# Optimization experiments

Hardware: AMD Instinct MI355X
Metric: run time of the kernel (lower is better)

## Reference

```python
import jax, jax.numpy as jnp
import numpy as np

BS, N, D, H = 4, 2048, 512, 8
DK = D // H
XAVIER_STD = float(np.sqrt(2.0 / (D + D)))  # xavier_normal_, gain=1


def setup_inputs() -> dict:
    key = jax.random.key(0)
    ks = jax.random.split(key, 10)
    Q = jax.random.normal(ks[0], (BS, N, D), jnp.float32)
    K = jax.random.normal(ks[1], (BS, N, D), jnp.float32)
    V = jax.random.normal(ks[2], (BS, N, D), jnp.float32)
    q_mas = jax.random.randint(ks[3], (BS, N, 1), 0, 2).astype(jnp.float32)
    k_mas = jax.random.randint(ks[4], (BS, N, 1), 0, 2).astype(jnp.float32)
    # 0/1 attention mask; force self-edges so no row is fully masked (avoids NaN softmax)
    att_mas = jax.random.randint(ks[5], (BS, N, N), 0, 2).astype(jnp.float32)
    att_mas = jnp.maximum(att_mas, jnp.eye(N, dtype=jnp.float32)[None])
    WQ = jax.random.normal(ks[6], (D, D), jnp.float32) * XAVIER_STD
    WK = jax.random.normal(ks[7], (D, D), jnp.float32) * XAVIER_STD
    WV = jax.random.normal(ks[8], (D, D), jnp.float32) * XAVIER_STD
    WO = jax.random.normal(ks[9], (D, D), jnp.float32) * XAVIER_STD
    return {"Q": Q, "K": K, "V": V, "q_mas": q_mas, "k_mas": k_mas,
            "att_mas": att_mas, "WQ": WQ, "WK": WK, "WV": WV, "WO": WO}


def reference(Q, K, V, q_mas, k_mas, att_mas, WQ, WK, WV, WO):
    bs, n, d = Q.shape
    h, dk = H, DK
    qm = q_mas.reshape(bs, 1, n, 1)  # (bs,1,n,1)
    km = k_mas.reshape(bs, 1, n, 1)
    # nn.Linear (no bias): x @ W.T ; split heads -> (bs,h,n,dk); apply pre-masks
    Qh = qm * (Q @ WQ.T).reshape(bs, n, h, dk).transpose(0, 2, 1, 3)
    Kh = km * (K @ WK.T).reshape(bs, n, h, dk).transpose(0, 2, 1, 3)
    Vh = km * (V @ WV.T).reshape(bs, n, h, dk).transpose(0, 2, 1, 3)
    scores = jnp.einsum('bhqd,bhkd->bhqk', Qh, Kh) / jnp.sqrt(jnp.float32(dk))
    mas = att_mas.reshape(bs, 1, n, n)
    scores = jnp.where(mas.astype(bool), scores, -jnp.inf)
    attn = jax.nn.softmax(scores, axis=-1) * mas
    y = jnp.einsum('bhqk,bhkd->bhqd', attn, Vh) * km  # post-mask (note: km over query dim, as in source)
    y = y.transpose(0, 2, 1, 3).reshape(bs, n, d)
    y = (y @ WO.T) * k_mas.reshape(bs, n, 1)
    return y
```

## Files before the change

kernel.cpp:

```cpp
#include <hip/hip_runtime.h>


#define BS_    4
#define NSEQ   2048
#define DMODEL 512
#define NH     8
#define DKH    64
#define MROWS  (BS_ * NSEQ)

typedef unsigned short ushort_t;
typedef __attribute__((ext_vector_type(8))) short short8;
typedef __attribute__((ext_vector_type(4))) float floatx4;

__device__ __forceinline__ ushort_t f2bf(float f) {
    unsigned int x = __builtin_bit_cast(unsigned int, f);
    return (ushort_t)((x + 0x8000u) >> 16);
}
__device__ __forceinline__ floatx4 mfma_bf16(short8 a, short8 b, floatx4 c) {
    return __builtin_amdgcn_mfma_f32_16x16x32_bf16(a, b, c, 0, 0, 0);
}
__device__ __forceinline__ void gld16(const ushort_t* g, ushort_t* l) {
    __builtin_amdgcn_global_load_lds(
        (const __attribute__((address_space(1))) unsigned int*)g,
        (__attribute__((address_space(3))) unsigned int*)l, 16, 0, 0);
}

__global__ __launch_bounds__(256) void cvt3_kernel(const float* __restrict__ a,
                                                   const float* __restrict__ b,
                                                   const float* __restrict__ c,
                                                   ushort_t* __restrict__ dst, int n4) {
    const float* src = (blockIdx.y == 0) ? a : (blockIdx.y == 1) ? b : c;
    ushort_t* d = dst + (size_t)blockIdx.y * ((size_t)n4 * 4);
    const int i = blockIdx.x * blockDim.x + threadIdx.x;
    const float4 v = ((const float4*)src)[i];
    ushort4 o;
    o.x = f2bf(v.x); o.y = f2bf(v.y); o.z = f2bf(v.z); o.w = f2bf(v.w);
    ((ushort4*)d)[i] = o;
}

__global__ __launch_bounds__(256) void cvt4_kernel(const float* __restrict__ a,
                                                   const float* __restrict__ b,
                                                   const float* __restrict__ c,
                                                   const float* __restrict__ e,
                                                   ushort_t* __restrict__ dst, int n4) {
    const float* src = (blockIdx.y == 0) ? a : (blockIdx.y == 1) ? b
                     : (blockIdx.y == 2) ? c : e;
    ushort_t* d = dst + (size_t)blockIdx.y * ((size_t)n4 * 4);
    const int i = blockIdx.x * blockDim.x + threadIdx.x;
    const float4 v = ((const float4*)src)[i];
    ushort4 o;
    o.x = f2bf(v.x); o.y = f2bf(v.y); o.z = f2bf(v.z); o.w = f2bf(v.w);
    ((ushort4*)d)[i] = o;
}

__global__ __launch_bounds__(256) void gemm_proj(const ushort_t* __restrict__ Xall,
                                                 const ushort_t* __restrict__ Wall,
                                                 const float* __restrict__ qmas,
                                                 const float* __restrict__ kmas,
                                                 ushort_t* __restrict__ Qh,
                                                 ushort_t* __restrict__ Kh,
                                                 ushort_t* __restrict__ Vt) {
    __shared__ ushort_t As[2][128 * 32];
    const int z = blockIdx.z;
    const ushort_t* X  = Xall + (size_t)z * MROWS * DMODEL;
    const ushort_t* Wb = Wall + (size_t)z * DMODEL * DMODEL;
    const float* rowmask = (z == 0) ? qmas : kmas;

    const int tid  = threadIdx.x;
    const int wave = tid >> 6;
    const int lane = tid & 63;
    const int l16  = lane & 15;
    const int quad = lane >> 4;
    const int wr   = wave >> 1;
    const int wc   = wave & 1;
    const int m0   = blockIdx.x * 128;
    const int n0   = blockIdx.y * 128;
    const int r4   = lane >> 2;
    const int p4   = lane & 3;

    floatx4 acc[4][4];
#pragma unroll
    for (int t = 0; t < 4; ++t)
#pragma unroll
        for (int u = 0; u < 4; ++u) acc[t][u] = (floatx4){0.f, 0.f, 0.f, 0.f};

    const ushort_t* Wrow[4];
#pragma unroll
    for (int u = 0; u < 4; ++u)
        Wrow[u] = Wb + (size_t)(n0 + wc * 64 + u * 16 + l16) * DMODEL + quad * 8;

    for (int k0 = 0; k0 < DMODEL; k0 += 64) {
#pragma unroll
        for (int i = 0; i < 4; ++i) {
            const int idx = wave * 4 + i;
            const int h = idx >> 3, rg = idx & 7;
            gld16(X + (size_t)(m0 + rg * 16 + r4) * DMODEL + k0 + h * 32 + p4 * 8,
                  &As[h][rg * 512]);
        }
        short8 bf[4][2];
#pragma unroll
        for (int u = 0; u < 4; ++u)
#pragma unroll
            for (int kc = 0; kc < 2; ++kc)
                bf[u][kc] = *(const short8*)(Wrow[u] + k0 + kc * 32);
        __syncthreads();
        short8 af[4][2];
#pragma unroll
        for (int t = 0; t < 4; ++t)
#pragma unroll
            for (int kc = 0; kc < 2; ++kc)
                af[t][kc] = *(const short8*)&As[kc][(wr * 64 + t * 16 + l16) * 32 + quad * 8];
#pragma unroll
        for (int t = 0; t < 4; ++t)
#pragma unroll
            for (int u = 0; u < 4; ++u) {
                acc[t][u] = mfma_bf16(af[t][0], bf[u][0], acc[t][u]);
                acc[t][u] = mfma_bf16(af[t][1], bf[u][1], acc[t][u]);
            }
        __syncthreads();
    }

    float rm[4][4];
#pragma unroll
    for (int t = 0; t < 4; ++t)
#pragma unroll
        for (int r = 0; r < 4; ++r)
            rm[t][r] = rowmask[m0 + wr * 64 + t * 16 + quad * 4 + r];

    const int bb    = m0 >> 11;
    const int nbase = (m0 & (NSEQ - 1)) + wr * 64;
#pragma unroll
    for (int t = 0; t < 4; ++t) {
#pragma unroll
        for (int u = 0; u < 4; ++u) {
            const int d = n0 + wc * 64 + u * 16 + l16;
            const int h = d >> 6, cc = d & 63;
            if (z < 2) {
                ushort_t* dst = (z == 0) ? Qh : Kh;
#pragma unroll
                for (int r = 0; r < 4; ++r) {
                    const int n = nbase + t * 16 + quad * 4 + r;
                    dst[((size_t)(bb * NH + h) * NSEQ + n) * DKH + cc] =
                        f2bf(acc[t][u][r] * rm[t][r]);
                }
            } else {
                ushort4 pk;
                pk.x = f2bf(acc[t][u][0] * rm[t][0]);
                pk.y = f2bf(acc[t][u][1] * rm[t][1]);
                pk.z = f2bf(acc[t][u][2] * rm[t][2]);
                pk.w = f2bf(acc[t][u][3] * rm[t][3]);
                const int n = nbase + t * 16 + quad * 4;
                *(ushort4*)(Vt + ((size_t)(bb * NH + h) * DKH + cc) * NSEQ + n) = pk;
            }
        }
    }
}

__global__ __launch_bounds__(256) void gemm_out(const ushort_t* __restrict__ X,
                                                const ushort_t* __restrict__ Wb,
                                                const float* __restrict__ rowmask,
                                                float* __restrict__ dst) {
    __shared__ ushort_t As[2][128 * 32];
    const int tid  = threadIdx.x;
    const int wave = tid >> 6;
    const int lane = tid & 63;
    const int l16  = lane & 15;
    const int quad = lane >> 4;
    const int wr   = wave >> 1;
    const int wc   = wave & 1;
    const int m0   = blockIdx.x * 128;
    const int n0   = blockIdx.y * 128;
    const int r4   = lane >> 2;
    const int p4   = lane & 3;

    floatx4 acc[4][4];
#pragma unroll
    for (int t = 0; t < 4; ++t)
#pragma unroll
        for (int u = 0; u < 4; ++u) acc[t][u] = (floatx4){0.f, 0.f, 0.f, 0.f};

    const ushort_t* Wrow[4];
#pragma unroll
    for (int u = 0; u < 4; ++u)
        Wrow[u] = Wb + (size_t)(n0 + wc * 64 + u * 16 + l16) * DMODEL + quad * 8;

    for (int k0 = 0; k0 < DMODEL; k0 += 64) {
#pragma unroll
        for (int i = 0; i < 4; ++i) {
            const int idx = wave * 4 + i;
            const int h = idx >> 3, rg = idx & 7;
            gld16(X + (size_t)(m0 + rg * 16 + r4) * DMODEL + k0 + h * 32 + p4 * 8,
                  &As[h][rg * 512]);
        }
        short8 bf[4][2];
#pragma unroll
        for (int u = 0; u < 4; ++u)
#pragma unroll
            for (int kc = 0; kc < 2; ++kc)
                bf[u][kc] = *(const short8*)(Wrow[u] + k0 + kc * 32);
        __syncthreads();
        short8 af[4][2];
#pragma unroll
        for (int t = 0; t < 4; ++t)
#pragma unroll
            for (int kc = 0; kc < 2; ++kc)
                af[t][kc] = *(const short8*)&As[kc][(wr * 64 + t * 16 + l16) * 32 + quad * 8];
#pragma unroll
        for (int t = 0; t < 4; ++t)
#pragma unroll
            for (int u = 0; u < 4; ++u) {
                acc[t][u] = mfma_bf16(af[t][0], bf[u][0], acc[t][u]);
                acc[t][u] = mfma_bf16(af[t][1], bf[u][1], acc[t][u]);
            }
        __syncthreads();
    }

#pragma unroll
    for (int t = 0; t < 4; ++t) {
#pragma unroll
        for (int r = 0; r < 4; ++r) {
            const int m = m0 + wr * 64 + t * 16 + quad * 4 + r;
            const float rm = rowmask[m];
#pragma unroll
            for (int u = 0; u < 4; ++u) {
                const int d = n0 + wc * 64 + u * 16 + l16;
                dst[(size_t)m * DMODEL + d] = acc[t][u][r] * rm;
            }
        }
    }
}

__global__ __launch_bounds__(256, 3) void attn_kernel(const ushort_t* __restrict__ Qh,
                                                      const ushort_t* __restrict__ Kh,
                                                      const ushort_t* __restrict__ Vt,
                                                      const float* __restrict__ amas,
                                                      const float* __restrict__ kmas,
                                                      ushort_t* __restrict__ y) {
    __shared__ ushort_t Ks[2][128 * 32];
    __shared__ ushort_t Vs[4][64 * 32];
    __shared__ ushort_t Ps[4][4][16 * 32];

    const int tid  = threadIdx.x;
    const int wave = tid >> 6;
    const int lane = tid & 63;
    const int l16  = lane & 15;
    const int quad = lane >> 4;
    const int r4   = lane >> 2;
    const int p4   = lane & 3;
    const int h    = blockIdx.y;
    const int b    = blockIdx.z;
    const int qw   = blockIdx.x * 64 + wave * 16;

    const ushort_t* Kb = Kh + (size_t)(b * NH + h) * NSEQ * DKH;
    const ushort_t* Vb = Vt + (size_t)(b * NH + h) * DKH * NSEQ;
    const float*    Am = amas + (size_t)(b * NSEQ + qw) * NSEQ;

    const ushort_t* Qp = Qh + ((size_t)((b * NH + h) * NSEQ) + qw + l16) * DKH + quad * 8;
    const short8 qfa = *(const short8*)Qp;
    const short8 qfb = *(const short8*)(Qp + 32);

    float lpart[4] = {0.f, 0.f, 0.f, 0.f};
    floatx4 accO[4];
#pragma unroll
    for (int ct = 0; ct < 4; ++ct) accO[ct] = (floatx4){0.f, 0.f, 0.f, 0.f};

    const float CEXP = 0.18033688011112042f;

    for (int kt = 0; kt < NSEQ / 128; ++kt) {
        const int k0 = kt * 128;

        __syncthreads();

        float av[8][4];
#pragma unroll
        for (int fr = 0; fr < 8; ++fr)
#pragma unroll
            for (int r = 0; r < 4; ++r)
                av[fr][r] = Am[(size_t)(quad * 4 + r) * NSEQ + k0 + fr * 16 + l16];

#pragma unroll
        for (int i = 0; i < 4; ++i) {
            const int idx = wave * 4 + i;
            const int hh = idx >> 3, rg = idx & 7;
            gld16(Kb + (size_t)(k0 + rg * 16 + r4) * DKH + hh * 32 + p4 * 8,
                  &Ks[hh][rg * 512]);
        }
#pragma unroll
        for (int i = 0; i < 4; ++i) {
            const int idx = wave * 4 + i;
            const int kf = idx >> 2, rg = idx & 3;
            gld16(Vb + (size_t)(rg * 16 + r4) * NSEQ + k0 + kf * 32 + p4 * 8,
                  &Vs[kf][rg * 512]);
        }
        __syncthreads();

        floatx4 S[8];
#pragma unroll
        for (int fr = 0; fr < 8; ++fr) {
            const short8 ka = *(const short8*)&Ks[0][(fr * 16 + l16) * 32 + quad * 8];
            const short8 kb = *(const short8*)&Ks[1][(fr * 16 + l16) * 32 + quad * 8];
            floatx4 s = {0.f, 0.f, 0.f, 0.f};
            s = mfma_bf16(qfa, ka, s);
            s = mfma_bf16(qfb, kb, s);
            S[fr] = s;
        }

#pragma unroll
        for (int fr = 0; fr < 8; ++fr) {
#pragma unroll
            for (int r = 0; r < 4; ++r) {
                const float p = av[fr][r] * exp2f(S[fr][r] * CEXP);
                lpart[r] += p;
                Ps[wave][fr >> 1][(quad * 4 + r) * 32 + (fr & 1) * 16 + l16] = f2bf(p);
            }
        }

        __builtin_amdgcn_wave_barrier();
        short8 pf[4];
#pragma unroll
        for (int kf = 0; kf < 4; ++kf)
            pf[kf] = *(const short8*)&Ps[wave][kf][l16 * 32 + quad * 8];
        __builtin_amdgcn_wave_barrier();

#pragma unroll
        for (int ct = 0; ct < 4; ++ct) {
#pragma unroll
            for (int kf = 0; kf < 4; ++kf) {
                const short8 vb = *(const short8*)&Vs[kf][(ct * 16 + l16) * 32 + quad * 8];
                accO[ct] = mfma_bf16(pf[kf], vb, accO[ct]);
            }
        }
    }

#pragma unroll
    for (int r = 0; r < 4; ++r) {
        float l = lpart[r];
        l += __shfl_xor(l, 1);
        l += __shfl_xor(l, 2);
        l += __shfl_xor(l, 4);
        l += __shfl_xor(l, 8);
        const int q = qw + quad * 4 + r;
        const float scale = kmas[b * NSEQ + q] / l;
#pragma unroll
        for (int ct = 0; ct < 4; ++ct) {
            y[(size_t)(b * NSEQ + q) * DMODEL + h * DKH + ct * 16 + l16] =
                f2bf(accO[ct][r] * scale);
        }
    }
}

extern "C" void kernel_launch(void* const* d_in, const int* in_sizes, int n_in,
                              void* d_out, int out_size, void* d_ws, size_t ws_size,
                              hipStream_t stream) {
    (void)in_sizes; (void)n_in; (void)out_size; (void)ws_size;
    const float* Q  = (const float*)d_in[0];
    const float* K  = (const float*)d_in[1];
    const float* V  = (const float*)d_in[2];
    const float* qm = (const float*)d_in[3];
    const float* km = (const float*)d_in[4];
    const float* am = (const float*)d_in[5];
    const float* WQ = (const float*)d_in[6];
    const float* WK = (const float*)d_in[7];
    const float* WV = (const float*)d_in[8];
    const float* WO = (const float*)d_in[9];

    const size_t XN = (size_t)MROWS * DMODEL;
    const size_t WN = (size_t)DMODEL * DMODEL;
    ushort_t* Xbf = (ushort_t*)d_ws;
    ushort_t* Wbf = Xbf + 3 * XN;
    ushort_t* WOb = Wbf + 3 * WN;
    ushort_t* Qh  = Wbf + 4 * WN;
    ushort_t* Kh  = Qh + XN;
    ushort_t* Vt  = Kh + XN;
    ushort_t* y   = Vt + XN;
    float* out = (float*)d_out;

    hipLaunchKernelGGL(cvt3_kernel, dim3(4096, 3), dim3(256), 0, stream,
                       Q, K, V, Xbf, (int)(XN / 4));
    hipLaunchKernelGGL(cvt4_kernel, dim3(256, 4), dim3(256), 0, stream,
                       WQ, WK, WV, WO, Wbf, (int)(WN / 4));

    hipLaunchKernelGGL(gemm_proj, dim3(MROWS / 128, DMODEL / 128, 3), dim3(256), 0, stream,
                       Xbf, Wbf, qm, km, Qh, Kh, Vt);

    hipLaunchKernelGGL(attn_kernel, dim3(NSEQ / 64, NH, BS_), dim3(256), 0, stream,
                       Qh, Kh, Vt, am, km, y);

    hipLaunchKernelGGL(gemm_out, dim3(MROWS / 128, DMODEL / 128), dim3(256), 0, stream,
                       y, WOb, km, out);
}
```

Before: 294.2 us.

## Bit-pack attention mask, merge conversion kernels, retile GEMMs with LDS-staged weights

A single prep kernel now does the bf16 conversions of inputs and weights and also packs the float attention mask into a 1-bit-per-entry bitmask using wave ballots. The attention kernel then reads 32x less mask data. It also swaps the MFMA operand order so each lane holds one query row, which allows packed bf16 P stores and a simpler row-sum reduction through LDS. The projection and output GEMMs move to 64x128 tiles with weights staged in LDS via global_load_lds, giving more blocks and less register pressure. The cost is one extra full pass over the float mask in the prep kernel.

```diff
diff --git a/kernel.cpp b/kernel.cpp
--- a/kernel.cpp
+++ b/kernel.cpp
@@ -7,6 +7,9 @@
 #define NH     8
 #define DKH    64
 #define MROWS  (BS_ * NSEQ)
+#define NW32   (NSEQ / 32)
+#define XN     ((size_t)MROWS * DMODEL)
+#define WN     ((size_t)DMODEL * DMODEL)
 
 typedef unsigned short ushort_t;
 typedef __attribute__((ext_vector_type(8))) short short8;
@@ -15,6 +18,11 @@
 __device__ __forceinline__ ushort_t f2bf(float f) {
     unsigned int x = __builtin_bit_cast(unsigned int, f);
     return (ushort_t)((x + 0x8000u) >> 16);
+}
+__device__ __forceinline__ unsigned int pack2bf(float lo, float hi) {
+    const unsigned int a = __builtin_bit_cast(unsigned int, lo) + 0x8000u;
+    const unsigned int b = __builtin_bit_cast(unsigned int, hi) + 0x8000u;
+    return __builtin_amdgcn_perm(b, a, 0x07060302u);
 }
 __device__ __forceinline__ floatx4 mfma_bf16(short8 a, short8 b, floatx4 c) {
     return __builtin_amdgcn_mfma_f32_16x16x32_bf16(a, b, c, 0, 0, 0);
@@ -25,33 +33,78 @@
         (__attribute__((address_space(3))) unsigned int*)l, 16, 0, 0);
 }
 
-__global__ __launch_bounds__(256) void cvt3_kernel(const float* __restrict__ a,
-                                                   const float* __restrict__ b,
-                                                   const float* __restrict__ c,
-                                                   ushort_t* __restrict__ dst, int n4) {
-    const float* src = (blockIdx.y == 0) ? a : (blockIdx.y == 1) ? b : c;
-    ushort_t* d = dst + (size_t)blockIdx.y * ((size_t)n4 * 4);
-    const int i = blockIdx.x * blockDim.x + threadIdx.x;
-    const float4 v = ((const float4*)src)[i];
-    ushort4 o;
-    o.x = f2bf(v.x); o.y = f2bf(v.y); o.z = f2bf(v.z); o.w = f2bf(v.w);
-    ((ushort4*)d)[i] = o;
-}
-
-__global__ __launch_bounds__(256) void cvt4_kernel(const float* __restrict__ a,
-                                                   const float* __restrict__ b,
-                                                   const float* __restrict__ c,
-                                                   const float* __restrict__ e,
-                                                   ushort_t* __restrict__ dst, int n4) {
-    const float* src = (blockIdx.y == 0) ? a : (blockIdx.y == 1) ? b
-                     : (blockIdx.y == 2) ? c : e;
-    ushort_t* d = dst + (size_t)blockIdx.y * ((size_t)n4 * 4);
-    const int i = blockIdx.x * blockDim.x + threadIdx.x;
-    const float4 v = ((const float4*)src)[i];
-    ushort4 o;
-    o.x = f2bf(v.x); o.y = f2bf(v.y); o.z = f2bf(v.z); o.w = f2bf(v.w);
-    ((ushort4*)d)[i] = o;
-}
+__global__ __launch_bounds__(256) void prep_kernel(const float* __restrict__ Q,
+                                                   const float* __restrict__ K,
+                                                   const float* __restrict__ V,
+                                                   const float* __restrict__ WQ,
+                                                   const float* __restrict__ WK,
+                                                   const float* __restrict__ WV,
+                                                   const float* __restrict__ WO,
+                                                   const float* __restrict__ am,
+                                                   ushort_t* __restrict__ Xbf,
+                                                   ushort_t* __restrict__ Wbf,
+                                                   unsigned int* __restrict__ pm) {
+    const int bx  = blockIdx.x;
+    const int tid = threadIdx.x;
+    if (bx < 12288) {
+        const int seg = bx >> 12;
+        const int i = (bx & 4095) * 256 + tid;
+        const float* src = (seg == 0) ? Q : (seg == 1) ? K : V;
+        const float4 v = ((const float4*)src)[i];
+        ushort4 o;
+        o.x = f2bf(v.x); o.y = f2bf(v.y); o.z = f2bf(v.z); o.w = f2bf(v.w);
+        ((ushort4*)(Xbf + (size_t)seg * XN))[i] = o;
+    } else if (bx < 13312) {
+        const int b2 = bx - 12288;
+        const int seg = b2 >> 8;
+        const int i = (b2 & 255) * 256 + tid;
+        const float* src = (seg == 0) ? WQ : (seg == 1) ? WK : (seg == 2) ? WV : WO;
+        const float4 v = ((const float4*)src)[i];
+        ushort4 o;
+        o.x = f2bf(v.x); o.y = f2bf(v.y); o.z = f2bf(v.z); o.w = f2bf(v.w);
+        ((ushort4*)(Wbf + (size_t)seg * WN))[i] = o;
+    } else {
+        const int gid = (bx - 13312) * 256 + tid;
+        const float v = am[gid];
+        const unsigned long long m = __ballot(v != 0.f);
+        if ((tid & 63) == 0) {
+            uint2 w; w.x = (unsigned int)m; w.y = (unsigned int)(m >> 32);
+            *(uint2*)&pm[gid >> 5] = w;
+        }
+    }
+}
+
+#define GEMM_V3_LOOP(X_, W_)                                                          \
+    floatx4 acc[2][4];                                                                \
+    _Pragma("unroll") for (int t = 0; t < 2; ++t)                                     \
+        _Pragma("unroll") for (int u = 0; u < 4; ++u)                                 \
+            acc[t][u] = (floatx4){0.f, 0.f, 0.f, 0.f};                                \
+    for (int k0 = 0; k0 < DMODEL; k0 += 64) {                                         \
+        _Pragma("unroll") for (int i = 0; i < 2; ++i) {                               \
+            const int ca = wave * 2 + i, mg = ca >> 1, kc = ca & 1;                   \
+            gld16(X_ + (size_t)(m0 + mg * 16 + r4) * DMODEL + k0 + kc * 32 + p4 * 8,  \
+                  &As[ca * 512]);                                                     \
+        }                                                                             \
+        _Pragma("unroll") for (int i = 0; i < 4; ++i) {                               \
+            const int cb = wave * 4 + i, ng = cb >> 1, kc = cb & 1;                   \
+            gld16(W_ + (size_t)(n0 + ng * 16 + r4) * DMODEL + k0 + kc * 32 + p4 * 8,  \
+                  &Bs[cb * 512]);                                                     \
+        }                                                                             \
+        __syncthreads();                                                              \
+        _Pragma("unroll") for (int kc = 0; kc < 2; ++kc) {                            \
+            short8 a[2], bfr[4];                                                      \
+            _Pragma("unroll") for (int t = 0; t < 2; ++t)                             \
+                a[t] = *(const short8*)&As[((wr * 2 + t) * 2 + kc) * 512 +            \
+                                           l16 * 32 + quad * 8];                      \
+            _Pragma("unroll") for (int u = 0; u < 4; ++u)                             \
+                bfr[u] = *(const short8*)&Bs[((wc * 4 + u) * 2 + kc) * 512 +          \
+                                             l16 * 32 + quad * 8];                    \
+            _Pragma("unroll") for (int t = 0; t < 2; ++t)                             \
+                _Pragma("unroll") for (int u = 0; u < 4; ++u)                         \
+                    acc[t][u] = mfma_bf16(a[t], bfr[u], acc[t][u]);                   \
+        }                                                                             \
+        __syncthreads();                                                              \
+    }
 
 __global__ __launch_bounds__(256) void gemm_proj(const ushort_t* __restrict__ Xall,
                                                  const ushort_t* __restrict__ Wall,
@@ -60,10 +113,11 @@
                                                  ushort_t* __restrict__ Qh,
                                                  ushort_t* __restrict__ Kh,
                                                  ushort_t* __restrict__ Vt) {
-    __shared__ ushort_t As[2][128 * 32];
+    __shared__ ushort_t As[8 * 512];
+    __shared__ ushort_t Bs[16 * 512];
     const int z = blockIdx.z;
-    const ushort_t* X  = Xall + (size_t)z * MROWS * DMODEL;
-    const ushort_t* Wb = Wall + (size_t)z * DMODEL * DMODEL;
+    const ushort_t* X  = Xall + (size_t)z * XN;
+    const ushort_t* Wb = Wall + (size_t)z * WN;
     const float* rowmask = (z == 0) ? qmas : kmas;
 
     const int tid  = threadIdx.x;
@@ -73,86 +127,49 @@
     const int quad = lane >> 4;
     const int wr   = wave >> 1;
     const int wc   = wave & 1;
-    const int m0   = blockIdx.x * 128;
+    const int m0   = blockIdx.x * 64;
     const int n0   = blockIdx.y * 128;
     const int r4   = lane >> 2;
     const int p4   = lane & 3;
 
-    floatx4 acc[4][4];
-#pragma unroll
-    for (int t = 0; t < 4; ++t)
-#pragma unroll
-        for (int u = 0; u < 4; ++u) acc[t][u] = (floatx4){0.f, 0.f, 0.f, 0.f};
-
-    const ushort_t* Wrow[4];
-#pragma unroll
-    for (int u = 0; u < 4; ++u)
-        Wrow[u] = Wb + (size_t)(n0 + wc * 64 + u * 16 + l16) * DMODEL + quad * 8;
-
-    for (int k0 = 0; k0 < DMODEL; k0 += 64) {
-#pragma unroll
-        for (int i = 0; i < 4; ++i) {
-            const int idx = wave * 4 + i;
-            const int h = idx >> 3, rg = idx & 7;
-            gld16(X + (size_t)(m0 + rg * 16 + r4) * DMODEL + k0 + h * 32 + p4 * 8,
-                  &As[h][rg * 512]);
-        }
-        short8 bf[4][2];
-#pragma unroll
-        for (int u = 0; u < 4; ++u)
-#pragma unroll
-            for (int kc = 0; kc < 2; ++kc)
-                bf[u][kc] = *(const short8*)(Wrow[u] + k0 + kc * 32);
-        __syncthreads();
-        short8 af[4][2];
-#pragma unroll
-        for (int t = 0; t < 4; ++t)
-#pragma unroll
-            for (int kc = 0; kc < 2; ++kc)
-                af[t][kc] = *(const short8*)&As[kc][(wr * 64 + t * 16 + l16) * 32 + quad * 8];
-#pragma unroll
-        for (int t = 0; t < 4; ++t)
-#pragma unroll
-            for (int u = 0; u < 4; ++u) {
-                acc[t][u] = mfma_bf16(af[t][0], bf[u][0], acc[t][u]);
-                acc[t][u] = mfma_bf16(af[t][1], bf[u][1], acc[t][u]);
-            }
-        __syncthreads();
-    }
-
-    float rm[4][4];
-#pragma unroll
-    for (int t = 0; t < 4; ++t)
+    GEMM_V3_LOOP(X, Wb)
+
+    float rm[2][4];
+#pragma unroll
+    for (int t = 0; t < 2; ++t)
 #pragma unroll
         for (int r = 0; r < 4; ++r)
-            rm[t][r] = rowmask[m0 + wr * 64 + t * 16 + quad * 4 + r];
+            rm[t][r] = rowmask[m0 + wr * 32 + t * 16 + quad * 4 + r];
 
     const int bb    = m0 >> 11;
-    const int nbase = (m0 & (NSEQ - 1)) + wr * 64;
-#pragma unroll
-    for (int t = 0; t < 4; ++t) {
-#pragma unroll
-        for (int u = 0; u < 4; ++u) {
-            const int d = n0 + wc * 64 + u * 16 + l16;
-            const int h = d >> 6, cc = d & 63;
-            if (z < 2) {
-                ushort_t* dst = (z == 0) ? Qh : Kh;
+    const int nbase = (m0 & (NSEQ - 1)) + wr * 32;
+    const int hh    = (n0 >> 6) + wc;
+
+    if (z < 2) {
+        ushort_t* dst = (z == 0) ? Qh : Kh;
+#pragma unroll
+        for (int t = 0; t < 2; ++t)
+#pragma unroll
+            for (int u = 0; u < 4; ++u)
 #pragma unroll
                 for (int r = 0; r < 4; ++r) {
                     const int n = nbase + t * 16 + quad * 4 + r;
-                    dst[((size_t)(bb * NH + h) * NSEQ + n) * DKH + cc] =
+                    dst[((size_t)(bb * NH + hh) * NSEQ + n) * DKH + u * 16 + l16] =
                         f2bf(acc[t][u][r] * rm[t][r]);
                 }
-            } else {
+    } else {
+#pragma unroll
+        for (int t = 0; t < 2; ++t)
+#pragma unroll
+            for (int u = 0; u < 4; ++u) {
                 ushort4 pk;
                 pk.x = f2bf(acc[t][u][0] * rm[t][0]);
                 pk.y = f2bf(acc[t][u][1] * rm[t][1]);
                 pk.z = f2bf(acc[t][u][2] * rm[t][2]);
                 pk.w = f2bf(acc[t][u][3] * rm[t][3]);
                 const int n = nbase + t * 16 + quad * 4;
-                *(ushort4*)(Vt + ((size_t)(bb * NH + h) * DKH + cc) * NSEQ + n) = pk;
+                *(ushort4*)(Vt + ((size_t)(bb * NH + hh) * DKH + u * 16 + l16) * NSEQ + n) = pk;
             }
-        }
     }
 }
 
@@ -160,7 +177,8 @@
                                                 const ushort_t* __restrict__ Wb,
                                                 const float* __restrict__ rowmask,
                                                 float* __restrict__ dst) {
-    __shared__ ushort_t As[2][128 * 32];
+    __shared__ ushort_t As[8 * 512];
+    __shared__ ushort_t Bs[16 * 512];
     const int tid  = threadIdx.x;
     const int wave = tid >> 6;
     const int lane = tid & 63;
@@ -168,77 +186,36 @@
     const int quad = lane >> 4;
     const int wr   = wave >> 1;
     const int wc   = wave & 1;
-    const int m0   = blockIdx.x * 128;
+    const int m0   = blockIdx.x * 64;
     const int n0   = blockIdx.y * 128;
     const int r4   = lane >> 2;
     const int p4   = lane & 3;
 
-    floatx4 acc[4][4];
-#pragma unroll
-    for (int t = 0; t < 4; ++t)
-#pragma unroll
-        for (int u = 0; u < 4; ++u) acc[t][u] = (floatx4){0.f, 0.f, 0.f, 0.f};
-
-    const ushort_t* Wrow[4];
-#pragma unroll
-    for (int u = 0; u < 4; ++u)
-        Wrow[u] = Wb + (size_t)(n0 + wc * 64 + u * 16 + l16) * DMODEL + quad * 8;
-
-    for (int k0 = 0; k0 < DMODEL; k0 += 64) {
-#pragma unroll
-        for (int i = 0; i < 4; ++i) {
-            const int idx = wave * 4 + i;
-            const int h = idx >> 3, rg = idx & 7;
-            gld16(X + (size_t)(m0 + rg * 16 + r4) * DMODEL + k0 + h * 32 + p4 * 8,
-                  &As[h][rg * 512]);
-        }
-        short8 bf[4][2];
-#pragma unroll
-        for (int u = 0; u < 4; ++u)
-#pragma unroll
-            for (int kc = 0; kc < 2; ++kc)
-                bf[u][kc] = *(const short8*)(Wrow[u] + k0 + kc * 32);
-        __syncthreads();
-        short8 af[4][2];
-#pragma unroll
-        for (int t = 0; t < 4; ++t)
-#pragma unroll
-            for (int kc = 0; kc < 2; ++kc)
-                af[t][kc] = *(const short8*)&As[kc][(wr * 64 + t * 16 + l16) * 32 + quad * 8];
-#pragma unroll
-        for (int t = 0; t < 4; ++t)
-#pragma unroll
-            for (int u = 0; u < 4; ++u) {
-                acc[t][u] = mfma_bf16(af[t][0], bf[u][0], acc[t][u]);
-                acc[t][u] = mfma_bf16(af[t][1], bf[u][1], acc[t][u]);
-            }
-        __syncthreads();
-    }
-
-#pragma unroll
-    for (int t = 0; t < 4; ++t) {
+    GEMM_V3_LOOP(X, Wb)
+
+#pragma unroll
+    for (int t = 0; t < 2; ++t)
 #pragma unroll
         for (int r = 0; r < 4; ++r) {
-            const int m = m0 + wr * 64 + t * 16 + quad * 4 + r;
+            const int m = m0 + wr * 32 + t * 16 + quad * 4 + r;
             const float rm = rowmask[m];
 #pragma unroll
-            for (int u = 0; u < 4; ++u) {
-                const int d = n0 + wc * 64 + u * 16 + l16;
-                dst[(size_t)m * DMODEL + d] = acc[t][u][r] * rm;
-            }
-        }
-    }
+            for (int u = 0; u < 4; ++u)
+                dst[(size_t)m * DMODEL + n0 + wc * 64 + u * 16 + l16] =
+                    acc[t][u][r] * rm;
+        }
 }
 
 __global__ __launch_bounds__(256, 3) void attn_kernel(const ushort_t* __restrict__ Qh,
                                                       const ushort_t* __restrict__ Kh,
                                                       const ushort_t* __restrict__ Vt,
-                                                      const float* __restrict__ amas,
+                                                      const unsigned int* __restrict__ pmask,
                                                       const float* __restrict__ kmas,
                                                       ushort_t* __restrict__ y) {
     __shared__ ushort_t Ks[2][128 * 32];
     __shared__ ushort_t Vs[4][64 * 32];
     __shared__ ushort_t Ps[4][4][16 * 32];
+    __shared__ float    Lrow[4][16];
 
     const int tid  = threadIdx.x;
     const int wave = tid >> 6;
@@ -253,13 +230,13 @@
 
     const ushort_t* Kb = Kh + (size_t)(b * NH + h) * NSEQ * DKH;
     const ushort_t* Vb = Vt + (size_t)(b * NH + h) * DKH * NSEQ;
-    const float*    Am = amas + (size_t)(b * NSEQ + qw) * NSEQ;
+    const unsigned int* Pm = pmask + (size_t)(b * NSEQ + qw) * NW32;
 
     const ushort_t* Qp = Qh + ((size_t)((b * NH + h) * NSEQ) + qw + l16) * DKH + quad * 8;
     const short8 qfa = *(const short8*)Qp;
     const short8 qfb = *(const short8*)(Qp + 32);
 
-    float lpart[4] = {0.f, 0.f, 0.f, 0.f};
+    float lsum = 0.f;
     floatx4 accO[4];
 #pragma unroll
     for (int ct = 0; ct < 4; ++ct) accO[ct] = (floatx4){0.f, 0.f, 0.f, 0.f};
@@ -271,12 +248,11 @@
 
         __syncthreads();
 
-        float av[8][4];
-#pragma unroll
-        for (int fr = 0; fr < 8; ++fr)
-#pragma unroll
-            for (int r = 0; r < 4; ++r)
-                av[fr][r] = Am[(size_t)(quad * 4 + r) * NSEQ + k0 + fr * 16 + l16];
+        unsigned int mwa[4];
+        {
+            const uint4 m4 = *(const uint4*)&Pm[(size_t)l16 * NW32 + kt * 4];
+            mwa[0] = m4.x; mwa[1] = m4.y; mwa[2] = m4.z; mwa[3] = m4.w;
+        }
 
 #pragma unroll
         for (int i = 0; i < 4; ++i) {
@@ -300,19 +276,26 @@
             const short8 ka = *(const short8*)&Ks[0][(fr * 16 + l16) * 32 + quad * 8];
             const short8 kb = *(const short8*)&Ks[1][(fr * 16 + l16) * 32 + quad * 8];
             floatx4 s = {0.f, 0.f, 0.f, 0.f};
-            s = mfma_bf16(qfa, ka, s);
-            s = mfma_bf16(qfb, kb, s);
+            s = mfma_bf16(ka, qfa, s);
+            s = mfma_bf16(kb, qfb, s);
             S[fr] = s;
         }
 
 #pragma unroll
         for (int fr = 0; fr < 8; ++fr) {
+            float p[4];
 #pragma unroll
             for (int r = 0; r < 4; ++r) {
-                const float p = av[fr][r] * exp2f(S[fr][r] * CEXP);
-                lpart[r] += p;
-                Ps[wave][fr >> 1][(quad * 4 + r) * 32 + (fr & 1) * 16 + l16] = f2bf(p);
+                const unsigned int bit =
+                    (mwa[fr >> 1] >> ((fr & 1) * 16 + quad * 4 + r)) & 1u;
+                const float e = exp2f(S[fr][r] * CEXP);
+                p[r] = bit ? e : 0.f;
+                lsum += p[r];
             }
+            uint2 w;
+            w.x = pack2bf(p[0], p[1]);
+            w.y = pack2bf(p[2], p[3]);
+            *(uint2*)&Ps[wave][fr >> 1][l16 * 32 + (fr & 1) * 16 + quad * 4] = w;
         }
 
         __builtin_amdgcn_wave_barrier();
@@ -332,15 +315,15 @@
         }
     }
 
+    lsum += __shfl_xor(lsum, 16);
+    lsum += __shfl_xor(lsum, 32);
+    if (lane < 16) Lrow[wave][lane] = lsum;
+    __builtin_amdgcn_wave_barrier();
+
 #pragma unroll
     for (int r = 0; r < 4; ++r) {
-        float l = lpart[r];
-        l += __shfl_xor(l, 1);
-        l += __shfl_xor(l, 2);
-        l += __shfl_xor(l, 4);
-        l += __shfl_xor(l, 8);
         const int q = qw + quad * 4 + r;
-        const float scale = kmas[b * NSEQ + q] / l;
+        const float scale = kmas[b * NSEQ + q] / Lrow[wave][quad * 4 + r];
 #pragma unroll
         for (int ct = 0; ct < 4; ++ct) {
             y[(size_t)(b * NSEQ + q) * DMODEL + h * DKH + ct * 16 + l16] =
@@ -364,8 +347,6 @@
     const float* WV = (const float*)d_in[8];
     const float* WO = (const float*)d_in[9];
 
-    const size_t XN = (size_t)MROWS * DMODEL;
-    const size_t WN = (size_t)DMODEL * DMODEL;
     ushort_t* Xbf = (ushort_t*)d_ws;
     ushort_t* Wbf = Xbf + 3 * XN;
     ushort_t* WOb = Wbf + 3 * WN;
@@ -373,19 +354,18 @@
     ushort_t* Kh  = Qh + XN;
     ushort_t* Vt  = Kh + XN;
     ushort_t* y   = Vt + XN;
+    unsigned int* pm = (unsigned int*)(y + XN);
     float* out = (float*)d_out;
 
-    hipLaunchKernelGGL(cvt3_kernel, dim3(4096, 3), dim3(256), 0, stream,
-                       Q, K, V, Xbf, (int)(XN / 4));
-    hipLaunchKernelGGL(cvt4_kernel, dim3(256, 4), dim3(256), 0, stream,
-                       WQ, WK, WV, WO, Wbf, (int)(WN / 4));
-
-    hipLaunchKernelGGL(gemm_proj, dim3(MROWS / 128, DMODEL / 128, 3), dim3(256), 0, stream,
+    hipLaunchKernelGGL(prep_kernel, dim3(78848), dim3(256), 0, stream,
+                       Q, K, V, WQ, WK, WV, WO, am, Xbf, Wbf, pm);
+
+    hipLaunchKernelGGL(gemm_proj, dim3(MROWS / 64, DMODEL / 128, 3), dim3(256), 0, stream,
                        Xbf, Wbf, qm, km, Qh, Kh, Vt);
 
     hipLaunchKernelGGL(attn_kernel, dim3(NSEQ / 64, NH, BS_), dim3(256), 0, stream,
-                       Qh, Kh, Vt, am, km, y);
-
-    hipLaunchKernelGGL(gemm_out, dim3(MROWS / 128, DMODEL / 128), dim3(256), 0, stream,
+                       Qh, Kh, Vt, pm, km, y);
+
+    hipLaunchKernelGGL(gemm_out, dim3(MROWS / 64, DMODEL / 128), dim3(256), 0, stream,
                        y, WOb, km, out);
 }
```

After: 303.8 us. 3.3% more time.
